# Optimization experiments

Measured on AMD Instinct MI355X. Metric: run time of the kernel, lower is better.

Reference implementation:

```python
import jax, jax.numpy as jnp
import numpy as np

B, C, H, W = 2, 512, 48, 48
HEADS = 8
REDUCTION = 4
DPH = max(C // REDUCTION // HEADS, 1)   # 16
TOTAL = DPH * HEADS                      # 128
EPS_NORM = 1e-12
EPS_BN = 1e-5


def setup_inputs() -> dict:
    key = jax.random.key(0)
    ks = jax.random.split(key, 6)
    x = jax.random.normal(ks[0], (B, C, H, W), dtype=jnp.float32)
    # 1x1 convs stored as [out_ch, in_ch] matrices
    w_qkv = jax.random.normal(ks[1], (3 * TOTAL, C), dtype=jnp.float32) * (1.0 / np.sqrt(C))
    w_out = jax.random.normal(ks[2], (C, TOTAL), dtype=jnp.float32) * (1.0 / np.sqrt(TOTAL))
    temperature = jnp.ones((HEADS, 1, 1), dtype=jnp.float32)
    bn_gamma = jnp.ones((C,), dtype=jnp.float32)
    bn_beta = jnp.zeros((C,), dtype=jnp.float32)
    return {"x": x, "w_qkv": w_qkv, "temperature": temperature,
            "w_out": w_out, "bn_gamma": bn_gamma, "bn_beta": bn_beta}


def _l2norm(t):
    # F.normalize(t, dim=-1): t / max(||t||_2, eps)
    n = jnp.sqrt(jnp.sum(t * t, axis=-1, keepdims=True))
    return t / jnp.maximum(n, EPS_NORM)


def reference(x, w_qkv, temperature, w_out, bn_gamma, bn_beta):
    b, c, h, w = x.shape
    n = h * w
    # qkv 1x1 conv: [b, 3*TOTAL, h, w]
    qkv = jnp.einsum('bchw,oc->bohw', x, w_qkv)
    q, k, v = jnp.split(qkv, 3, axis=1)
    # [b, heads, dph, n] -> [b, heads, n, dph]
    def heads_tokens(t):
        return t.reshape(b, HEADS, DPH, n).transpose(0, 1, 3, 2)
    q = _l2norm(heads_tokens(q))
    k = _l2norm(heads_tokens(k))
    v = heads_tokens(v)
    # [b, heads, n, n]
    attn = jnp.einsum('bhnd,bhmd->bhnm', q, k) * temperature[None]
    attn = jax.nn.softmax(attn, axis=-1)
    out = jnp.einsum('bhnm,bhmd->bhnd', attn, v)          # [b, heads, n, dph]
    out = out.transpose(0, 1, 3, 2).reshape(b, TOTAL, h, w)
    # project_out: 1x1 conv then BatchNorm2d (training-mode batch stats)
    out = jnp.einsum('bthw,ct->bchw', out, w_out)
    mean = jnp.mean(out, axis=(0, 2, 3))
    var = jnp.mean((out - mean[None, :, None, None]) ** 2, axis=(0, 2, 3))
    out = (out - mean[None, :, None, None]) * jax.lax.rsqrt(var + EPS_BN)[None, :, None, None]
    out = out * bn_gamma[None, :, None, None] + bn_beta[None, :, None, None]
    return out
```

## Files before the change

kernel.cpp:

```cpp
#include <hip/hip_runtime.h>

#define NB 2
#define CC 512
#define NN 2304
#define NH 8
#define DD 16
#define TT 128
#define O3 384

typedef __attribute__((ext_vector_type(4))) float f32x4;
typedef __attribute__((ext_vector_type(8))) __bf16 bf16x8;
typedef __attribute__((ext_vector_type(4))) __bf16 bf16x4;
typedef __attribute__((ext_vector_type(4))) _Float16 f16x4;

__global__ __launch_bounds__(256) void k0_convert(
    const float* __restrict__ x, const float* __restrict__ wqkv,
    const float* __restrict__ wout,
    __bf16* __restrict__ xT, __bf16* __restrict__ wqb, __bf16* __restrict__ wob)
{
    int bid = blockIdx.x;
    int t = threadIdx.x;
    if (bid < 576) {
        __shared__ float tile[64][65];
        int b = bid / 288, rem = bid % 288;
        int nt = rem / 8, cb = rem % 8;
        int n0 = nt * 64, c0 = cb * 64;
        int tc = t >> 6, tn = t & 63;
#pragma unroll
        for (int i = 0; i < 16; i++) {
            int cl = i * 4 + tc;
            tile[cl][tn] = x[(size_t)(b * CC + c0 + cl) * NN + n0 + tn];
        }
        __syncthreads();
#pragma unroll
        for (int i = 0; i < 16; i++) {
            int nl = i * 4 + tc;
            xT[(size_t)(b * NN + n0 + nl) * CC + c0 + tn] = (__bf16)tile[tn][nl];
        }
    } else {
        int wid = bid - 576;
        int base = wid * 256 + t;
#pragma unroll
        for (int i = 0; i < 16; i++) {
            int j = base + i * 16384;
            if (j < O3 * CC) wqb[j] = (__bf16)wqkv[j];
            else             wob[j - O3 * CC] = (__bf16)wout[j - O3 * CC];
        }
    }
}

__global__ __launch_bounds__(256) void k1_qkv(
    const __bf16* __restrict__ xT, const __bf16* __restrict__ wqb,
    _Float16* __restrict__ Q, _Float16* __restrict__ K, _Float16* __restrict__ VT)
{
    int ob = blockIdx.x, nt = blockIdx.y, b = blockIdx.z;
    int lane = threadIdx.x & 63, wave = threadIdx.x >> 6;
    int quad = lane >> 4, col = lane & 15;
    int n0 = nt * 64 + wave * 16;
    int o0 = ob * 32;

    f32x4 acc[2];
    acc[0] = (f32x4){0.f, 0.f, 0.f, 0.f};
    acc[1] = (f32x4){0.f, 0.f, 0.f, 0.f};

    const __bf16* arow = xT + (size_t)(b * NN + n0 + col) * CC + quad * 8;
    const __bf16* brow0 = wqb + (size_t)(o0 + col) * CC + quad * 8;
    const __bf16* brow1 = brow0 + 16 * CC;

    bf16x8 a  = *(const bf16x8*)(arow);
    bf16x8 w0 = *(const bf16x8*)(brow0);
    bf16x8 w1 = *(const bf16x8*)(brow1);
#pragma unroll
    for (int ks = 0; ks < 16; ks++) {
        bf16x8 an, wn0, wn1;
        if (ks < 15) {
            an  = *(const bf16x8*)(arow + (ks + 1) * 32);
            wn0 = *(const bf16x8*)(brow0 + (ks + 1) * 32);
            wn1 = *(const bf16x8*)(brow1 + (ks + 1) * 32);
        }
        acc[0] = __builtin_amdgcn_mfma_f32_16x16x32_bf16(a, w0, acc[0], 0, 0, 0);
        acc[1] = __builtin_amdgcn_mfma_f32_16x16x32_bf16(a, w1, acc[1], 0, 0, 0);
        a = an; w0 = wn0; w1 = wn1;
    }

#pragma unroll
    for (int s = 0; s < 2; s++) {
        int oc = o0 + s * 16 + col;
        int d = oc & 15, h = (oc >> 4) & 7, kind = oc >> 7;
        f32x4 v = acc[s];
        if (kind < 2) {
            float ss0 = v[0] * v[0], ss1 = v[1] * v[1], ss2 = v[2] * v[2], ss3 = v[3] * v[3];
#pragma unroll
            for (int m = 1; m < 16; m <<= 1) {
                ss0 += __shfl_xor(ss0, m);
                ss1 += __shfl_xor(ss1, m);
                ss2 += __shfl_xor(ss2, m);
                ss3 += __shfl_xor(ss3, m);
            }
            v[0] *= 1.0f / fmaxf(sqrtf(ss0), 1e-12f);
            v[1] *= 1.0f / fmaxf(sqrtf(ss1), 1e-12f);
            v[2] *= 1.0f / fmaxf(sqrtf(ss2), 1e-12f);
            v[3] *= 1.0f / fmaxf(sqrtf(ss3), 1e-12f);
            _Float16* dst = (kind == 0 ? Q : K) + (size_t)(b * NH + h) * NN * DD;
#pragma unroll
            for (int r = 0; r < 4; r++) {
                int n = n0 + quad * 4 + r;
                dst[(size_t)n * DD + d] = (_Float16)v[r];
            }
        } else {
            f16x4 pk;
#pragma unroll
            for (int r = 0; r < 4; r++) pk[r] = (_Float16)v[r];
            int n = n0 + quad * 4;
            *(f16x4*)(VT + (size_t)((b * NH + h) * DD + d) * NN + n) = pk;
        }
    }
}

__global__ __launch_bounds__(256) void k2_attn(
    const _Float16* __restrict__ Q, const _Float16* __restrict__ K,
    const _Float16* __restrict__ VT, const float* __restrict__ temp,
    float* __restrict__ Opart, float* __restrict__ Lpart)
{
    int qt = blockIdx.x, bh = blockIdx.y, sp = blockIdx.z;
    int lane = threadIdx.x & 63, wave = threadIdx.x >> 6;
    int quad = lane >> 4, col = lane & 15;
    int kbase = sp * 288;
    int qbase = qt * 256 + wave * 64;

    const _Float16* Qb = Q + (size_t)bh * NN * DD;
    float tl2 = temp[bh & 7] * 1.4426950408889634f;

    f16x4 qf0 = *(const f16x4*)(Qb + (size_t)(qbase +  0 + col) * DD + quad * 4);
    f16x4 qf1 = *(const f16x4*)(Qb + (size_t)(qbase + 16 + col) * DD + quad * 4);
    f16x4 qf2 = *(const f16x4*)(Qb + (size_t)(qbase + 32 + col) * DD + quad * 4);
    f16x4 qf3 = *(const f16x4*)(Qb + (size_t)(qbase + 48 + col) * DD + quad * 4);

    f32x4 oa0 = {0.f,0.f,0.f,0.f}, oa1 = {0.f,0.f,0.f,0.f};
    f32x4 oa2 = {0.f,0.f,0.f,0.f}, oa3 = {0.f,0.f,0.f,0.f};
    float la0 = 0.f, la1 = 0.f, la2 = 0.f, la3 = 0.f;
    const f32x4 zc = {0.f,0.f,0.f,0.f};

    const _Float16* kp = K + (size_t)bh * NN * DD + (size_t)(kbase + col) * DD + quad * 4;
    const _Float16* vp = VT + (size_t)bh * DD * NN + (size_t)col * NN + kbase + quad * 4;

    f16x4 kfa = *(const f16x4*)(kp);
    f16x4 kfb = *(const f16x4*)(kp + 16 * DD);
    f16x4 vfa = *(const f16x4*)(vp);
    f16x4 vfb = *(const f16x4*)(vp + 16);

#define K2_CHUNK(KF, VF)                                                        \
    {                                                                           \
        f32x4 s0 = __builtin_amdgcn_mfma_f32_16x16x16f16(KF, qf0, zc, 0, 0, 0); \
        f32x4 s1 = __builtin_amdgcn_mfma_f32_16x16x16f16(KF, qf1, zc, 0, 0, 0); \
        f32x4 s2 = __builtin_amdgcn_mfma_f32_16x16x16f16(KF, qf2, zc, 0, 0, 0); \
        f32x4 s3 = __builtin_amdgcn_mfma_f32_16x16x16f16(KF, qf3, zc, 0, 0, 0); \
        f16x4 p0, p1, p2, p3;                                                   \
        _Pragma("unroll")                                                       \
        for (int r = 0; r < 4; ++r) {                                           \
            float e0 = __builtin_amdgcn_exp2f(tl2 * s0[r]);                     \
            float e1 = __builtin_amdgcn_exp2f(tl2 * s1[r]);                     \
            float e2 = __builtin_amdgcn_exp2f(tl2 * s2[r]);                     \
            float e3 = __builtin_amdgcn_exp2f(tl2 * s3[r]);                     \
            p0[r] = (_Float16)e0; la0 += e0;                                    \
            p1[r] = (_Float16)e1; la1 += e1;                                    \
            p2[r] = (_Float16)e2; la2 += e2;                                    \
            p3[r] = (_Float16)e3; la3 += e3;                                    \
        }                                                                       \
        oa0 = __builtin_amdgcn_mfma_f32_16x16x16f16(VF, p0, oa0, 0, 0, 0);      \
        oa1 = __builtin_amdgcn_mfma_f32_16x16x16f16(VF, p1, oa1, 0, 0, 0);      \
        oa2 = __builtin_amdgcn_mfma_f32_16x16x16f16(VF, p2, oa2, 0, 0, 0);      \
        oa3 = __builtin_amdgcn_mfma_f32_16x16x16f16(VF, p3, oa3, 0, 0, 0);      \
    }

    for (int g = 0; g < 9; ++g) {
        f16x4 kna, knb, vna, vnb;
        if (g < 8) {
            kna = *(const f16x4*)(kp + 32 * DD);
            knb = *(const f16x4*)(kp + 48 * DD);
            vna = *(const f16x4*)(vp + 32);
            vnb = *(const f16x4*)(vp + 48);
        }
        K2_CHUNK(kfa, vfa)
        K2_CHUNK(kfb, vfb)
        kfa = kna; kfb = knb; vfa = vna; vfb = vnb;
        kp += 32 * DD; vp += 32;
    }
#undef K2_CHUNK

    la0 += __shfl_xor(la0, 16); la0 += __shfl_xor(la0, 32);
    la1 += __shfl_xor(la1, 16); la1 += __shfl_xor(la1, 32);
    la2 += __shfl_xor(la2, 16); la2 += __shfl_xor(la2, 32);
    la3 += __shfl_xor(la3, 16); la3 += __shfl_xor(la3, 32);

    float* Ob = Opart + (((size_t)sp * 16 + bh) * DD + quad * 4) * NN + qbase + col;
#pragma unroll
    for (int r = 0; r < 4; ++r) {
        Ob[(size_t)r * NN +  0] = oa0[r];
        Ob[(size_t)r * NN + 16] = oa1[r];
        Ob[(size_t)r * NN + 32] = oa2[r];
        Ob[(size_t)r * NN + 48] = oa3[r];
    }
    float lv = (quad == 0) ? la0 : (quad == 1) ? la1 : (quad == 2) ? la2 : la3;
    Lpart[((size_t)sp * 16 + bh) * NN + qbase + quad * 16 + col] = lv;
}

__global__ __launch_bounds__(256) void k2c_combine(
    const float* __restrict__ Opart, const float* __restrict__ Lpart,
    __bf16* __restrict__ AO)
{
    int gid = blockIdx.x * 256 + threadIdx.x;
    int bh = gid / NN, n = gid % NN;
    int b = bh >> 3, h = bh & 7;
    float l = 0.f;
#pragma unroll
    for (int sp = 0; sp < 8; sp++)
        l += Lpart[((size_t)sp * 16 + bh) * NN + n];
    float inv = 1.0f / l;
    float o[16];
#pragma unroll
    for (int d = 0; d < 16; d++) o[d] = 0.f;
#pragma unroll
    for (int sp = 0; sp < 8; sp++) {
        const float* Ob = Opart + ((size_t)sp * 16 + bh) * DD * NN + n;
#pragma unroll
        for (int d = 0; d < 16; d++) o[d] += Ob[(size_t)d * NN];
    }
    bf16x8 v0, v1;
#pragma unroll
    for (int d = 0; d < 8; d++) v0[d] = (__bf16)(o[d] * inv);
#pragma unroll
    for (int d = 0; d < 8; d++) v1[d] = (__bf16)(o[d + 8] * inv);
    __bf16* dst = AO + (size_t)b * NN * TT + (size_t)n * TT + h * DD;
    *(bf16x8*)dst = v0;
    *(bf16x8*)(dst + 8) = v1;
}

__global__ __launch_bounds__(256) void k3_proj(
    const __bf16* __restrict__ AO, const __bf16* __restrict__ wob,
    float* __restrict__ out)
{
    int cb = blockIdx.x, nt = blockIdx.y, b = blockIdx.z;
    int lane = threadIdx.x & 63, wave = threadIdx.x >> 6;
    int quad = lane >> 4, col = lane & 15;
    int n0 = nt * 64 + wave * 16, c0 = cb * 32;

    f32x4 acc[2];
    acc[0] = (f32x4){0.f, 0.f, 0.f, 0.f};
    acc[1] = (f32x4){0.f, 0.f, 0.f, 0.f};

    const __bf16* ab = AO + (size_t)(b * NN + n0 + col) * TT + quad * 8;
    const __bf16* wb0 = wob + (size_t)(c0 + col) * TT + quad * 8;
    const __bf16* wb1 = wb0 + 16 * TT;
#pragma unroll
    for (int ks = 0; ks < 4; ks++) {
        bf16x8 a  = *(const bf16x8*)(ab + ks * 32);
        bf16x8 w0 = *(const bf16x8*)(wb0 + ks * 32);
        bf16x8 w1 = *(const bf16x8*)(wb1 + ks * 32);
        acc[0] = __builtin_amdgcn_mfma_f32_16x16x32_bf16(a, w0, acc[0], 0, 0, 0);
        acc[1] = __builtin_amdgcn_mfma_f32_16x16x32_bf16(a, w1, acc[1], 0, 0, 0);
    }
#pragma unroll
    for (int s = 0; s < 2; s++) {
        int c = c0 + s * 16 + col;
        float* dst = out + (size_t)(b * CC + c) * NN + n0 + quad * 4;
        *(f32x4*)dst = acc[s];
    }
}

__global__ __launch_bounds__(256) void k4_bn(
    float* __restrict__ out, const float* __restrict__ gamma,
    const float* __restrict__ beta)
{
    int c = blockIdx.x;
    int t = threadIdx.x;
    float vals[18];
    float s = 0.f, q = 0.f;
#pragma unroll
    for (int i = 0; i < 18; i++) {
        int j = i * 256 + t;
        int b = j / NN, n = j % NN;
        float v = out[(size_t)(b * CC + c) * NN + n];
        vals[i] = v; s += v; q += v * v;
    }
#pragma unroll
    for (int m = 1; m < 64; m <<= 1) { s += __shfl_xor(s, m); q += __shfl_xor(q, m); }
    __shared__ float rs[4], rq[4];
    int lane = t & 63, wave = t >> 6;
    if (lane == 0) { rs[wave] = s; rq[wave] = q; }
    __syncthreads();
    s = rs[0] + rs[1] + rs[2] + rs[3];
    q = rq[0] + rq[1] + rq[2] + rq[3];
    float mean = s * (1.0f / 4608.0f);
    float var = q * (1.0f / 4608.0f) - mean * mean;
    float sc = rsqrtf(var + 1e-5f) * gamma[c];
    float sh = beta[c] - mean * sc;
#pragma unroll
    for (int i = 0; i < 18; i++) {
        int j = i * 256 + t;
        int b = j / NN, n = j % NN;
        out[(size_t)(b * CC + c) * NN + n] = vals[i] * sc + sh;
    }
}

extern "C" void kernel_launch(void* const* d_in, const int* in_sizes, int n_in,
                              void* d_out, int out_size, void* d_ws, size_t ws_size,
                              hipStream_t stream) {
    const float* x     = (const float*)d_in[0];
    const float* wqkv  = (const float*)d_in[1];
    const float* temp  = (const float*)d_in[2];
    const float* wout  = (const float*)d_in[3];
    const float* gamma = (const float*)d_in[4];
    const float* beta  = (const float*)d_in[5];
    float* out = (float*)d_out;

    char* ws = (char*)d_ws;
    const size_t OFF_XT = 0;
    const size_t OFF_WQ = 4718592;
    const size_t OFF_WO = 5111808;
    const size_t OFF_Q  = 5242880;
    const size_t OFF_K  = 6422528;
    const size_t OFF_VT = 7602176;
    const size_t OFF_AO = 8781824;
    const size_t OFF_OP = 9961472;
    const size_t OFF_LP = 28835840;

    __bf16* xT  = (__bf16*)(ws + OFF_XT);
    __bf16* wqb = (__bf16*)(ws + OFF_WQ);
    __bf16* wob = (__bf16*)(ws + OFF_WO);
    _Float16* Q  = (_Float16*)(ws + OFF_Q);
    _Float16* K  = (_Float16*)(ws + OFF_K);
    _Float16* VT = (_Float16*)(ws + OFF_VT);
    __bf16* AO  = (__bf16*)(ws + OFF_AO);
    float* Opart = (float*)(ws + OFF_OP);
    float* Lpart = (float*)(ws + OFF_LP);

    k0_convert<<<640, 256, 0, stream>>>(x, wqkv, wout, xT, wqb, wob);
    k1_qkv<<<dim3(12, 36, 2), 256, 0, stream>>>(xT, wqb, Q, K, VT);
    k2_attn<<<dim3(9, 16, 8), 256, 0, stream>>>(Q, K, VT, temp, Opart, Lpart);
    k2c_combine<<<144, 256, 0, stream>>>(Opart, Lpart, AO);
    k3_proj<<<dim3(16, 36, 2), 256, 0, stream>>>(AO, wob, out);
    k4_bn<<<512, 256, 0, stream>>>(out, gamma, beta);
}
```

Baseline: 141.4 us.

## Fuse split-K attention combine into attention kernel via shared-memory reduction

The attention kernel now launches 512-thread blocks in which each of 8 waves handles one key split for the same 64 queries. Partial outputs and row sums are reduced in shared memory and written directly as bf16 to AO. This removes the global Opart/Lpart round trip (about 19 MB of fp32 partials) and the separate combine kernel launch. In exchange, the grid shrinks to 576 larger blocks, the 36 KB of shared memory may reduce occupancy, and the final stores are scattered 2-element bf16 writes.

Result: faster. 138.2 us (-2.3%).

```diff
diff --git a/kernel.cpp b/kernel.cpp
--- a/kernel.cpp
+++ b/kernel.cpp
@@ -117,16 +117,19 @@
     }
 }
 
-__global__ __launch_bounds__(256) void k2_attn(
+__global__ __launch_bounds__(512) void k2_attn(
     const _Float16* __restrict__ Q, const _Float16* __restrict__ K,
     const _Float16* __restrict__ VT, const float* __restrict__ temp,
-    float* __restrict__ Opart, float* __restrict__ Lpart)
-{
-    int qt = blockIdx.x, bh = blockIdx.y, sp = blockIdx.z;
+    __bf16* __restrict__ AO)
+{
+    __shared__ float Osh[8][16][64];
+    __shared__ float Lsh[8][64];
+
+    int qt = blockIdx.x, bh = blockIdx.y;
     int lane = threadIdx.x & 63, wave = threadIdx.x >> 6;
     int quad = lane >> 4, col = lane & 15;
-    int kbase = sp * 288;
-    int qbase = qt * 256 + wave * 64;
+    int kbase = wave * 288;
+    int qbase = qt * 64;
 
     const _Float16* Qb = Q + (size_t)bh * NN * DD;
     float tl2 = temp[bh & 7] * 1.4426950408889634f;
@@ -193,47 +196,33 @@
     la2 += __shfl_xor(la2, 16); la2 += __shfl_xor(la2, 32);
     la3 += __shfl_xor(la3, 16); la3 += __shfl_xor(la3, 32);
 
-    float* Ob = Opart + (((size_t)sp * 16 + bh) * DD + quad * 4) * NN + qbase + col;
 #pragma unroll
     for (int r = 0; r < 4; ++r) {
-        Ob[(size_t)r * NN +  0] = oa0[r];
-        Ob[(size_t)r * NN + 16] = oa1[r];
-        Ob[(size_t)r * NN + 32] = oa2[r];
-        Ob[(size_t)r * NN + 48] = oa3[r];
+        Osh[wave][quad * 4 + r][ 0 + col] = oa0[r];
+        Osh[wave][quad * 4 + r][16 + col] = oa1[r];
+        Osh[wave][quad * 4 + r][32 + col] = oa2[r];
+        Osh[wave][quad * 4 + r][48 + col] = oa3[r];
     }
     float lv = (quad == 0) ? la0 : (quad == 1) ? la1 : (quad == 2) ? la2 : la3;
-    Lpart[((size_t)sp * 16 + bh) * NN + qbase + quad * 16 + col] = lv;
-}
-
-__global__ __launch_bounds__(256) void k2c_combine(
-    const float* __restrict__ Opart, const float* __restrict__ Lpart,
-    __bf16* __restrict__ AO)
-{
-    int gid = blockIdx.x * 256 + threadIdx.x;
-    int bh = gid / NN, n = gid % NN;
+    Lsh[wave][quad * 16 + col] = lv;
+    __syncthreads();
+
+    int t = threadIdx.x;
+    int q = t & 63, dg = t >> 6;
+    float l = 0.f;
+#pragma unroll
+    for (int w = 0; w < 8; ++w) l += Lsh[w][q];
+    float inv = 1.0f / l;
+    float o0 = 0.f, o1 = 0.f;
+#pragma unroll
+    for (int w = 0; w < 8; ++w) {
+        o0 += Osh[w][dg * 2 + 0][q];
+        o1 += Osh[w][dg * 2 + 1][q];
+    }
     int b = bh >> 3, h = bh & 7;
-    float l = 0.f;
-#pragma unroll
-    for (int sp = 0; sp < 8; sp++)
-        l += Lpart[((size_t)sp * 16 + bh) * NN + n];
-    float inv = 1.0f / l;
-    float o[16];
-#pragma unroll
-    for (int d = 0; d < 16; d++) o[d] = 0.f;
-#pragma unroll
-    for (int sp = 0; sp < 8; sp++) {
-        const float* Ob = Opart + ((size_t)sp * 16 + bh) * DD * NN + n;
-#pragma unroll
-        for (int d = 0; d < 16; d++) o[d] += Ob[(size_t)d * NN];
-    }
-    bf16x8 v0, v1;
-#pragma unroll
-    for (int d = 0; d < 8; d++) v0[d] = (__bf16)(o[d] * inv);
-#pragma unroll
-    for (int d = 0; d < 8; d++) v1[d] = (__bf16)(o[d + 8] * inv);
-    __bf16* dst = AO + (size_t)b * NN * TT + (size_t)n * TT + h * DD;
-    *(bf16x8*)dst = v0;
-    *(bf16x8*)(dst + 8) = v1;
+    __bf16* dst = AO + (size_t)(b * NN + qbase + q) * TT + h * DD + dg * 2;
+    dst[0] = (__bf16)(o0 * inv);
+    dst[1] = (__bf16)(o1 * inv);
 }
 
 __global__ __launch_bounds__(256) void k3_proj(
@@ -322,8 +311,6 @@
     const size_t OFF_K  = 6422528;
     const size_t OFF_VT = 7602176;
     const size_t OFF_AO = 8781824;
-    const size_t OFF_OP = 9961472;
-    const size_t OFF_LP = 28835840;
 
     __bf16* xT  = (__bf16*)(ws + OFF_XT);
     __bf16* wqb = (__bf16*)(ws + OFF_WQ);
@@ -332,13 +319,10 @@
     _Float16* K  = (_Float16*)(ws + OFF_K);
     _Float16* VT = (_Float16*)(ws + OFF_VT);
     __bf16* AO  = (__bf16*)(ws + OFF_AO);
-    float* Opart = (float*)(ws + OFF_OP);
-    float* Lpart = (float*)(ws + OFF_LP);
 
     k0_convert<<<640, 256, 0, stream>>>(x, wqkv, wout, xT, wqb, wob);
     k1_qkv<<<dim3(12, 36, 2), 256, 0, stream>>>(xT, wqb, Q, K, VT);
-    k2_attn<<<dim3(9, 16, 8), 256, 0, stream>>>(Q, K, VT, temp, Opart, Lpart);
-    k2c_combine<<<144, 256, 0, stream>>>(Opart, Lpart, AO);
+    k2_attn<<<dim3(36, 16), 512, 0, stream>>>(Q, K, VT, temp, AO);
     k3_proj<<<dim3(16, 36, 2), 256, 0, stream>>>(AO, wob, out);
     k4_bn<<<512, 256, 0, stream>>>(out, gamma, beta);
 }
```
